# Kernel tuning notes

Measured on AMD Instinct MI355X. Metric: run time of the kernel, lower is better.

Reference implementation:

```python
import jax, jax.numpy as jnp
import numpy as np

T_TRACK = 256   # tracklets per graph
M_DET = 256     # detections per graph
N_NODES = T_TRACK + M_DET
D_IN = 512      # raw node feature dim (stand-in for CNN crop features)
D_EMB = 256     # node embedding dim
SLACK = 0.2
LAM = 5.0
SINK_ITERS = 8


def box_iou(a, b):
    # a, b: [E,4] boxes (x1,y1,x2,y2)
    ix1 = jnp.maximum(a[:, 0], b[:, 0])
    iy1 = jnp.maximum(a[:, 1], b[:, 1])
    ix2 = jnp.minimum(a[:, 2], b[:, 2])
    iy2 = jnp.minimum(a[:, 3], b[:, 3])
    inter = jnp.clip(ix2 - ix1, 0.0) * jnp.clip(iy2 - iy1, 0.0)
    area_a = (a[:, 2] - a[:, 0]) * (a[:, 3] - a[:, 1])
    area_b = (b[:, 2] - b[:, 0]) * (b[:, 3] - b[:, 1])
    return inter / (area_a + area_b - inter + 1e-8)


def mlp2(x, W1, b1, W2, b2):
    return jax.nn.sigmoid(jax.nn.relu(x @ W1 + b1) @ W2 + b2)


def setup_inputs() -> dict:
    key = jax.random.key(0)
    ks = jax.random.split(key, 16)
    x = jax.random.normal(ks[0], (N_NODES, D_IN), jnp.float32)
    coords = jax.random.uniform(ks[1], (N_NODES, 4), jnp.float32)
    # valid boxes: x1<x2, y1<y2
    c = jax.random.uniform(ks[2], (N_NODES, 2), jnp.float32) * 100.0
    wh = jax.random.uniform(ks[3], (N_NODES, 2), jnp.float32) * 20.0 + 1.0
    coords_original = jnp.concatenate([c, c + wh], axis=1)
    # bipartite edges: track i (node i) <-> det j (node T_TRACK+j), both directions;
    # first T*M edges satisfy src < dst (the half kept by the row<col mask)
    src = jnp.repeat(jnp.arange(T_TRACK, dtype=jnp.int32), M_DET)
    dst = jnp.tile(jnp.arange(M_DET, dtype=jnp.int32) + T_TRACK, T_TRACK)
    edge_index = jnp.stack([jnp.concatenate([src, dst]), jnp.concatenate([dst, src])])
    s = 0.05
    p = lambda k, shp: jax.random.normal(k, shp, jnp.float32) * s
    return dict(
        x=x, coords=coords, coords_original=coords_original, edge_index=edge_index,
        W_cnn=p(ks[4], (D_IN, D_EMB)), b_cnn=jnp.zeros((D_EMB,), jnp.float32),
        Wapp1=p(ks[5], (2 * D_EMB, 128)), bapp1=jnp.zeros((128,), jnp.float32),
        Wapp2=p(ks[6], (128, 1)), bapp2=jnp.zeros((1,), jnp.float32),
        Wg1=p(ks[7], (8, 32)), bg1=jnp.zeros((32,), jnp.float32),
        Wg2=p(ks[8], (32, 1)), bg2=jnp.zeros((1,), jnp.float32),
        Wa1=p(ks[9], (2, 8)), ba1=jnp.zeros((8,), jnp.float32),
        Wa2=p(ks[10], (8, 1)), ba2=jnp.zeros((1,), jnp.float32),
        Wo1=p(ks[11], (D_EMB, D_EMB)), Wo2=p(ks[12], (D_EMB, D_EMB)),
        bo=jnp.zeros((D_EMB,), jnp.float32),
        Wf1=p(ks[13], (2, 8)), bf1=jnp.zeros((8,), jnp.float32),
        Wf2=p(ks[14], (8, 1)), bf2=jnp.zeros((1,), jnp.float32),
    )


def reference(x, coords, coords_original, edge_index, W_cnn, b_cnn, Wapp1, bapp1, Wapp2, bapp2, Wg1, bg1, Wg2, bg2, Wa1, ba1, Wa2, ba2, Wo1, Wo2, bo, Wf1, bf1, Wf2, bf2):
    src, dst = edge_index[0], edge_index[1]
    h = jax.nn.relu(x @ W_cnn + b_cnn)                      # [N, D]
    # per-edge appearance / geometry affinities (vectorized over all edges)
    app = mlp2(jnp.concatenate([h[src], h[dst]], 1), Wapp1, bapp1, Wapp2, bapp2)[:, 0]
    geo = mlp2(jnp.concatenate([coords[src], coords[dst]], 1), Wg1, bg1, Wg2, bg2)[:, 0]
    iou = box_iou(coords_original[src], coords_original[dst])
    e = mlp2(jnp.stack([app, geo], -1), Wa1, ba1, Wa2, ba2)[:, 0]   # [E]
    # message passing (optimNet): edge-gated neighbor aggregation
    agg = jax.ops.segment_sum(e[:, None] * h[src], dst, num_segments=N_NODES)
    out = jax.nn.relu(h @ Wo1 + agg @ Wo2 + bo)             # [N, D]
    # directed (src < dst) half of the edges only
    eh = T_TRACK * M_DET
    a, b = out[src[:eh]], out[dst[:eh]]
    na = jnp.maximum(jnp.linalg.norm(a, axis=-1), 1e-6)
    nb = jnp.maximum(jnp.linalg.norm(b, axis=-1), 1e-6)
    cos = jnp.sum(a * b, -1) / (na * nb)
    score = mlp2(jnp.stack([cos, iou[:eh]], -1), Wf1, bf1, Wf2, bf2)[:, 0]
    # assignment matrix with slack row/col, Sinkhorn normalization
    slack_v = jnp.exp(jnp.float32(LAM * SLACK))
    mat = jnp.full((T_TRACK + 1, M_DET + 1), slack_v, jnp.float32)
    mat = mat.at[:T_TRACK, :M_DET].set(jnp.exp(LAM * score).reshape(T_TRACK, M_DET))
    for _ in range(SINK_ITERS):
        mat = mat / jnp.sum(mat, axis=1, keepdims=True)
        mat = mat / jnp.sum(mat, axis=0, keepdims=True)
    return mat[:T_TRACK, :M_DET].reshape(-1)                # [T*M]
```

## Files before the change

### kernel.cpp

```cpp
#include <hip/hip_runtime.h>
#include <math.h>


__device__ __forceinline__ float sigmoidf_(float x) { return 1.0f / (1.0f + expf(-x)); }

typedef _Float16 h2t __attribute__((ext_vector_type(2)));

__device__ __forceinline__ h2t pack2(float x, float y) {
  h2t r; r.x = (_Float16)x; r.y = (_Float16)y; return r;
}
__device__ __forceinline__ float fdot2f(h2t a, h2t b, float c) {
  return __builtin_amdgcn_fdot2(a, b, c, false);
}
template <int CTRL>
__device__ __forceinline__ float dpp_get(float x) {
  return __builtin_bit_cast(
      float, __builtin_amdgcn_mov_dpp(__builtin_bit_cast(int, x), CTRL, 0xF, 0xF, false));
}
template <int IMM>
__device__ __forceinline__ float swz_get(float x) {
  return __builtin_bit_cast(
      float, __builtin_amdgcn_ds_swizzle(__builtin_bit_cast(int, x), IMM));
}
__device__ __forceinline__ float allred16(float x) {
  x += dpp_get<0xB1>(x);
  x += dpp_get<0x4E>(x);
  x += dpp_get<0x141>(x);
  x += dpp_get<0x140>(x);
  return x;
}

#define G_LOAD(T, AREG, BARR, AP, BP, LDB)                             \
  {                                                                    \
    AREG = *reinterpret_cast<const float4*>((AP) + (T) * 32);          \
    _Pragma("unroll") for (int kk = 0; kk < 32; ++kk)                  \
        BARR[kk] = (BP)[((T) * 32 + kk) * (LDB)];                      \
  }
#define G_STORE(BUF, AREG)                                             \
  {                                                                    \
    Ast[BUF][ac + 0][ar] = AREG.x; Ast[BUF][ac + 1][ar] = AREG.y;      \
    Ast[BUF][ac + 2][ar] = AREG.z; Ast[BUF][ac + 3][ar] = AREG.w;      \
  }
#define G_COMP(BUF, BARR)                                              \
  {                                                                    \
    _Pragma("unroll") for (int kk = 0; kk < 32; ++kk) {                \
      const float4 a4 =                                                \
          *reinterpret_cast<const float4*>(&Ast[BUF][kk][4 * ty]);     \
      const float bv = BARR[kk];                                       \
      acc[0] = fmaf(a4.x, bv, acc[0]); acc[1] = fmaf(a4.y, bv, acc[1]);\
      acc[2] = fmaf(a4.z, bv, acc[2]); acc[3] = fmaf(a4.w, bv, acc[3]);\
    }                                                                  \
  }

__global__ __launch_bounds__(256)
void k1_h(const float* __restrict__ x, const float* __restrict__ Wc,
          float* __restrict__ hAB) {
  __shared__ __align__(16) float Ast[2][32][36];
  const int tid = threadIdx.x;
  const int tx = tid & 31, ty = tid >> 5;
  const int ar = tid >> 3, ac = (tid & 7) * 4;
  const int bm = blockIdx.y * 32, bn = blockIdx.x * 32;
  const int z = blockIdx.z;
  const float* __restrict__ Bp = Wc + (z * 256) * 256 + bn + tx;
  const float* __restrict__ Ap = x + (bm + ar) * 512 + z * 256 + ac;
  float* __restrict__ Cout = hAB + z * 131072;
  float4 aA, aB;
  float bA[32], bB[32];
  float acc[4] = {0.f, 0.f, 0.f, 0.f};

  G_LOAD(0, aA, bA, Ap, Bp, 256);
  G_STORE(0, aA);
  __syncthreads();
  for (int t = 0; t < 8; t += 2) {
    G_LOAD(t + 1, aB, bB, Ap, Bp, 256);
    G_COMP(0, bA);
    G_STORE(1, aB);
    __syncthreads();
    if (t + 2 < 8) { G_LOAD(t + 2, aA, bA, Ap, Bp, 256); }
    G_COMP(1, bB);
    if (t + 2 < 8) { G_STORE(0, aA); }
    __syncthreads();
  }
#pragma unroll
  for (int i = 0; i < 4; ++i)
    Cout[(bm + 4 * ty + i) * 256 + bn + tx] = acc[i];
}

__global__ __launch_bounds__(256)
void k2_pqgw(const float* __restrict__ hAB, const float* __restrict__ bc,
             const float* __restrict__ W1, const float* __restrict__ b1,
             const float* __restrict__ Wo2, const float* __restrict__ Wo1,
             float* __restrict__ PQGW, float* __restrict__ PT) {
  __shared__ __align__(16) float Ast[2][32][36];
  const int tid = threadIdx.x;
  const int tx = tid & 31, ty = tid >> 5;
  const int ar = tid >> 3, ac = (tid & 7) * 4;
  const int bm = blockIdx.y * 32, bn = blockIdx.x * 32;
  const int col = bn + tx;
  const float* __restrict__ Bp;
  int ldb;
  if (bn < 128)       { Bp = W1 + col; ldb = 128; }
  else if (bn < 256)  { Bp = W1 + 256 * 128 + (col - 128); ldb = 128; }
  else if (bn < 512)  { Bp = Wo2 + (col - 256); ldb = 256; }
  else                { Bp = Wo1 + (col - 512); ldb = 256; }
  const float* __restrict__ ApA = hAB + (bm + ar) * 256 + ac;
  const float* __restrict__ ApB = ApA + 131072;
  const float* __restrict__ bcp = bc + ac;
  float4 aA, aB;
  float bA[32], bB[32];
  float acc[4] = {0.f, 0.f, 0.f, 0.f};

#define K2_LOAD(T, AREG, BARR)                                         \
  {                                                                    \
    const float4 xa = *reinterpret_cast<const float4*>(ApA + (T) * 32);\
    const float4 xb = *reinterpret_cast<const float4*>(ApB + (T) * 32);\
    const float4 xc = *reinterpret_cast<const float4*>(bcp + (T) * 32);\
    AREG.x = fmaxf(xa.x + xb.x + xc.x, 0.f);                           \
    AREG.y = fmaxf(xa.y + xb.y + xc.y, 0.f);                           \
    AREG.z = fmaxf(xa.z + xb.z + xc.z, 0.f);                           \
    AREG.w = fmaxf(xa.w + xb.w + xc.w, 0.f);                           \
    _Pragma("unroll") for (int kk = 0; kk < 32; ++kk)                  \
        BARR[kk] = Bp[((T) * 32 + kk) * ldb];                          \
  }

  K2_LOAD(0, aA, bA);
  G_STORE(0, aA);
  __syncthreads();
  for (int t = 0; t < 8; t += 2) {
    K2_LOAD(t + 1, aB, bB);
    G_COMP(0, bA);
    G_STORE(1, aB);
    __syncthreads();
    if (t + 2 < 8) { K2_LOAD(t + 2, aA, bA); }
    G_COMP(1, bB);
    if (t + 2 < 8) { G_STORE(0, aA); }
    __syncthreads();
  }
  if (bn < 128) {
    const float bias = b1[col];
#pragma unroll
    for (int i = 0; i < 4; ++i)
      PT[col * 512 + bm + 4 * ty + i] = acc[i] + bias;
  } else {
#pragma unroll
    for (int i = 0; i < 4; ++i)
      PQGW[(bm + 4 * ty + i) * 768 + col] = acc[i];
  }
#undef K2_LOAD
}

__global__ __launch_bounds__(256)
void k34_edges_out(const float* __restrict__ PQGW, const float* __restrict__ PT,
                   const float* __restrict__ coords, const float* __restrict__ Wapp2,
                   const float* __restrict__ bapp2, const float* __restrict__ Wg1,
                   const float* __restrict__ bg1, const float* __restrict__ Wg2,
                   const float* __restrict__ bg2, const float* __restrict__ Wa1,
                   const float* __restrict__ ba1, const float* __restrict__ Wa2,
                   const float* __restrict__ ba2, const float* __restrict__ bo,
                   float* __restrict__ outm, float* __restrict__ nrm) {
  __shared__ __align__(16) float2 qw[128];
  __shared__ __align__(16) float sWg1[256], sWg2[32], sGfix[32];
  __shared__ __align__(16) float sE[256];
  __shared__ float sWa1[16], sBa1[8], sWa2[8], wpart[4];
  const int tid = threadIdx.x;
  const int b = blockIdx.x;
  const bool istrack = (b < 256);
  const int vbase = istrack ? 256 : 0;

  if (tid < 128) {
    float2 t2;
    t2.x = PQGW[b * 768 + 128 + tid];
    t2.y = Wapp2[tid];
    qw[tid] = t2;
  }
  sWg1[tid] = Wg1[tid];
  if (tid < 32) sWg2[tid] = Wg2[tid];
  if (tid < 16) sWa1[tid] = Wa1[tid];
  if (tid < 8) { sBa1[tid] = ba1[tid]; sWa2[tid] = Wa2[tid]; }
  __syncthreads();
  if (tid < 32) {
    float g = bg1[tid];
#pragma unroll
    for (int q = 0; q < 4; ++q)
      g = fmaf(coords[b * 4 + q], sWg1[(4 + q) * 32 + tid], g);
    sGfix[tid] = g;
  }
  __syncthreads();

  const int vr = vbase + tid;
  const float* __restrict__ ptb = PT + vr;
  float z = 0.f;
#pragma unroll 8
  for (int j = 0; j < 128; ++j) {
    const float2 q2 = qw[j];
    float a = ptb[j * 512] + q2.x;
    a = a > 0.f ? a : 0.f;
    z = fmaf(a, q2.y, z);
  }
  const float app = sigmoidf_(z + bapp2[0]);
  const float4 cp = *reinterpret_cast<const float4*>(coords + vr * 4);
  float gz = 0.f;
#pragma unroll
  for (int m = 0; m < 32; ++m) {
    float hm = sGfix[m];
    hm = fmaf(cp.x, sWg1[0 * 32 + m], hm);
    hm = fmaf(cp.y, sWg1[1 * 32 + m], hm);
    hm = fmaf(cp.z, sWg1[2 * 32 + m], hm);
    hm = fmaf(cp.w, sWg1[3 * 32 + m], hm);
    hm = hm > 0.f ? hm : 0.f;
    gz = fmaf(hm, sWg2[m], gz);
  }
  const float geo = sigmoidf_(gz + bg2[0]);
  float ez = 0.f;
#pragma unroll
  for (int m = 0; m < 8; ++m) {
    float hm = fmaf(app, sWa1[m], fmaf(geo, sWa1[8 + m], sBa1[m]));
    hm = hm > 0.f ? hm : 0.f;
    ez = fmaf(hm, sWa2[m], ez);
  }
  sE[tid] = sigmoidf_(ez + ba2[0]);
  __syncthreads();

  const int c = tid;
  float a0 = 0.f, a1 = 0.f, a2 = 0.f, a3 = 0.f;
  const float* __restrict__ gcol = PQGW + vbase * 768 + 256 + c;
#pragma unroll 4
  for (int j = 0; j < 256; j += 4) {
    const float4 e4 = *reinterpret_cast<const float4*>(&sE[j]);
    a0 = fmaf(e4.x, gcol[(j + 0) * 768], a0);
    a1 = fmaf(e4.y, gcol[(j + 1) * 768], a1);
    a2 = fmaf(e4.z, gcol[(j + 2) * 768], a2);
    a3 = fmaf(e4.w, gcol[(j + 3) * 768], a3);
  }
  const float base = PQGW[b * 768 + 512 + c] + bo[c];
  float vv = base + ((a0 + a1) + (a2 + a3));
  vv = vv > 0.f ? vv : 0.f;
  outm[b * 256 + c] = vv;
  float nsq = vv * vv;
  nsq = allred16(nsq);
  nsq += swz_get<0x401F>(nsq);
  nsq += __shfl_xor(nsq, 32, 64);
  if ((tid & 63) == 0) wpart[tid >> 6] = nsq;
  __syncthreads();
  if (tid == 0)
    nrm[b] = fmaxf(sqrtf(wpart[0] + wpart[1] + wpart[2] + wpart[3]), 1e-6f);
}

__global__ __launch_bounds__(256)
void k6_score(const float* __restrict__ outm, const float* __restrict__ nrm,
              const float* __restrict__ co, const float* __restrict__ Wf1,
              const float* __restrict__ bf1, const float* __restrict__ Wf2,
              const float* __restrict__ bf2, float* __restrict__ Mblk) {
  __shared__ __align__(16) float Ast[2][32][36];
  const int tid = threadIdx.x;
  const int tx = tid & 31, ty = tid >> 5;
  const int ar = tid >> 3, ac = (tid & 7) * 4;
  const int s0 = blockIdx.y * 32, d0 = blockIdx.x * 32;
  const float* __restrict__ Ap = outm + (s0 + ar) * 256 + ac;
  const float* __restrict__ Bp = outm + (256 + d0 + tx) * 256;
  float4 aA, aB;
  float bA[32], bB[32];
  float acc[4] = {0.f, 0.f, 0.f, 0.f};

  G_LOAD(0, aA, bA, Ap, Bp, 1);
  G_STORE(0, aA);
  __syncthreads();
  for (int t = 0; t < 8; t += 2) {
    G_LOAD(t + 1, aB, bB, Ap, Bp, 1);
    G_COMP(0, bA);
    G_STORE(1, aB);
    __syncthreads();
    if (t + 2 < 8) { G_LOAD(t + 2, aA, bA, Ap, Bp, 1); }
    G_COMP(1, bB);
    if (t + 2 < 8) { G_STORE(0, aA); }
    __syncthreads();
  }
  const float nb = nrm[256 + d0 + tx];
  const float4 B4 = *reinterpret_cast<const float4*>(co + (256 + d0 + tx) * 4);
  const float areaB = (B4.z - B4.x) * (B4.w - B4.y);
  float w1c[8], w1i[8], w2[8];
#pragma unroll
  for (int m = 0; m < 8; ++m) {
    w1c[m] = Wf1[m]; w1i[m] = Wf1[8 + m]; w2[m] = Wf2[m];
  }
  const float bf20 = bf2[0];
#pragma unroll
  for (int i = 0; i < 4; ++i) {
    const int r = s0 + 4 * ty + i;
    const float4 A4 = *reinterpret_cast<const float4*>(co + r * 4);
    const float ix1 = fmaxf(A4.x, B4.x), iy1 = fmaxf(A4.y, B4.y);
    const float ix2 = fminf(A4.z, B4.z), iy2 = fminf(A4.w, B4.w);
    const float inter = fmaxf(ix2 - ix1, 0.f) * fmaxf(iy2 - iy1, 0.f);
    const float areaA = (A4.z - A4.x) * (A4.w - A4.y);
    const float i1 = inter / (areaA + areaB - inter + 1e-8f);
    const float cosv = acc[i] / (nrm[r] * nb);
    float sz = 0.f;
#pragma unroll
    for (int m = 0; m < 8; ++m) {
      float hm = fmaf(cosv, w1c[m], fmaf(i1, w1i[m], bf1[m]));
      hm = hm > 0.f ? hm : 0.f;
      sz = fmaf(hm, w2[m], sz);
    }
    const float score = sigmoidf_(sz + bf20);
    Mblk[r * 256 + d0 + tx] = expf(5.0f * score);
  }
}

__global__ __launch_bounds__(1024)
void k7_sink(const float* __restrict__ Mg, float* __restrict__ outp) {
  __shared__ __align__(16) float su_f[256];
  __shared__ __align__(16) float svs_f[256];
  __shared__ __align__(16) float psum[16][260];
  __shared__ float wsumU[16], wsumV[4];
  const int tid = threadIdx.x, w = tid >> 6, l = tid & 63;
  const float slack = 2.71828182845904523536f;
  const float INV256 = 0.00390625f;
  const int rev = ((l & 1) << 3) | ((l & 2) << 1) | ((l & 4) >> 1) | ((l & 8) >> 3);
  const bool b0 = l & 1, b1 = l & 2, b2 = l & 4, b3 = l & 8;

  h2t mrA[16], mrB[16];
#pragma unroll
  for (int i = 0; i < 16; ++i) {
    const float4 f = *reinterpret_cast<const float4*>(Mg + (w * 16 + i) * 256 + 4 * l);
    mrA[i] = pack2(f.x, f.y);
    mrB[i] = pack2(f.z, f.w);
  }
  if (tid < 256) svs_f[tid] = 256.0f;
  __syncthreads();

  float sv256 = 1.0f;
  for (int it = 0; it < 8; ++it) {
    const float sv_tot =
        (it == 0) ? 257.0f : (wsumV[0] + wsumV[1] + wsumV[2] + wsumV[3] + sv256);
    const float su256 = 1.0f / (slack * sv_tot);
    const float4 va = *reinterpret_cast<const float4*>(&svs_f[4 * l]);
    const h2t sva = pack2(va.x, va.y), svb = pack2(va.z, va.w);
    float p[16];
#pragma unroll
    for (int i = 0; i < 16; ++i) p[i] = fdot2f(mrA[i], sva, fdot2f(mrB[i], svb, 0.0f));
#pragma unroll
    for (int i = 0; i < 8; ++i) {
      const float keep = b0 ? p[i + 8] : p[i], give = b0 ? p[i] : p[i + 8];
      p[i] = keep + dpp_get<0xB1>(give);
    }
#pragma unroll
    for (int i = 0; i < 4; ++i) {
      const float keep = b1 ? p[i + 4] : p[i], give = b1 ? p[i] : p[i + 4];
      p[i] = keep + dpp_get<0x4E>(give);
    }
#pragma unroll
    for (int i = 0; i < 2; ++i) {
      const float keep = b2 ? p[i + 2] : p[i], give = b2 ? p[i] : p[i + 2];
      p[i] = keep + dpp_get<0x141>(give);
    }
    {
      const float keep = b3 ? p[1] : p[0], give = b3 ? p[0] : p[1];
      p[0] = keep + dpp_get<0x140>(give);
    }
    float S = p[0];
    S += swz_get<0x401F>(S);
    S += __shfl_xor(S, 32, 64);
    const float su_val = 1.0f / (S * INV256 + slack * sv256);
    if (l < 16) su_f[w * 16 + rev] = su_val;
    const float wsU = allred16(su_val);
    if (l == 0) wsumU[w] = wsU;
    asm volatile("s_waitcnt lgkmcnt(0)" ::: "memory");
    float su16[16];
#pragma unroll
    for (int k = 0; k < 16; k += 4) {
      const float4 t = *reinterpret_cast<const float4*>(&su_f[w * 16 + k]);
      su16[k] = t.x; su16[k + 1] = t.y; su16[k + 2] = t.z; su16[k + 3] = t.w;
    }
    float pc0 = 0.f, pc1 = 0.f, pc2 = 0.f, pc3 = 0.f;
#pragma unroll
    for (int i = 0; i < 16; ++i) {
      const float ui = su16[i];
      pc0 = fmaf((float)mrA[i].x, ui, pc0);
      pc1 = fmaf((float)mrA[i].y, ui, pc1);
      pc2 = fmaf((float)mrB[i].x, ui, pc2);
      pc3 = fmaf((float)mrB[i].y, ui, pc3);
    }
    float4 pcv; pcv.x = pc0; pcv.y = pc1; pcv.z = pc2; pcv.w = pc3;
    *reinterpret_cast<float4*>(&psum[w][4 * l]) = pcv;
    __syncthreads();
    const float su_tot = wsumU[0] + wsumU[1] + wsumU[2] + wsumU[3] + wsumU[4] +
                         wsumU[5] + wsumU[6] + wsumU[7] + wsumU[8] + wsumU[9] +
                         wsumU[10] + wsumU[11] + wsumU[12] + wsumU[13] +
                         wsumU[14] + wsumU[15] + su256;
    if (tid < 256) {
      float cs = 0.f;
#pragma unroll
      for (int g = 0; g < 16; ++g) cs += psum[g][tid];
      const float sv_val = 1.0f / (cs + slack * su256);
      svs_f[tid] = 256.0f * sv_val;
      float t = allred16(sv_val);
      t += swz_get<0x401F>(t);
      t += __shfl_xor(t, 32, 64);
      if (l == 0) wsumV[w] = t;
    }
    sv256 = 1.0f / (slack * su_tot);
    __syncthreads();
  }
  const float4 sv4 = *reinterpret_cast<const float4*>(&svs_f[4 * l]);
#pragma unroll
  for (int i = 0; i < 16; ++i) {
    const float uo = su_f[w * 16 + i] * INV256;
    float4 o;
    o.x = uo * (float)mrA[i].x * sv4.x;
    o.y = uo * (float)mrA[i].y * sv4.y;
    o.z = uo * (float)mrB[i].x * sv4.z;
    o.w = uo * (float)mrB[i].y * sv4.w;
    *reinterpret_cast<float4*>(outp + (w * 16 + i) * 256 + 4 * l) = o;
  }
}

extern "C" void kernel_launch(void* const* d_in, const int* in_sizes, int n_in,
                              void* d_out, int out_size, void* d_ws, size_t ws_size,
                              hipStream_t stream) {
  (void)in_sizes; (void)n_in; (void)out_size; (void)ws_size;
  const float* x      = (const float*)d_in[0];
  const float* coords = (const float*)d_in[1];
  const float* co     = (const float*)d_in[2];
  const float* Wc    = (const float*)d_in[4];
  const float* bc    = (const float*)d_in[5];
  const float* Wapp1 = (const float*)d_in[6];
  const float* bapp1 = (const float*)d_in[7];
  const float* Wapp2 = (const float*)d_in[8];
  const float* bapp2 = (const float*)d_in[9];
  const float* Wg1   = (const float*)d_in[10];
  const float* bg1   = (const float*)d_in[11];
  const float* Wg2   = (const float*)d_in[12];
  const float* bg2   = (const float*)d_in[13];
  const float* Wa1   = (const float*)d_in[14];
  const float* ba1   = (const float*)d_in[15];
  const float* Wa2   = (const float*)d_in[16];
  const float* ba2   = (const float*)d_in[17];
  const float* Wo1   = (const float*)d_in[18];
  const float* Wo2   = (const float*)d_in[19];
  const float* bo    = (const float*)d_in[20];
  const float* Wf1   = (const float*)d_in[21];
  const float* bf1   = (const float*)d_in[22];
  const float* Wf2   = (const float*)d_in[23];
  const float* bf2   = (const float*)d_in[24];

  float* ws   = (float*)d_ws;
  float* hAB  = ws + 0;
  float* PQGW = ws + 262144;
  float* PT   = ws + 655360;
  float* outm = ws + 720896;
  float* nrm  = ws + 851968;
  float* Mblk = ws + 852480;

  k1_h<<<dim3(8, 16, 2), 256, 0, stream>>>(x, Wc, hAB);
  k2_pqgw<<<dim3(24, 16), 256, 0, stream>>>(hAB, bc, Wapp1, bapp1, Wo2, Wo1,
                                            PQGW, PT);
  k34_edges_out<<<512, 256, 0, stream>>>(PQGW, PT, coords, Wapp2, bapp2, Wg1,
                                         bg1, Wg2, bg2, Wa1, ba1, Wa2, ba2, bo,
                                         outm, nrm);
  k6_score<<<dim3(8, 8), 256, 0, stream>>>(outm, nrm, co, Wf1, bf1, Wf2, bf2,
                                           Mblk);
  k7_sink<<<1, 1024, 0, stream>>>(Mblk, (float*)d_out);
}
```

Baseline: 88.66 us.

## Fuse edge/out and score kernels with per-node release/acquire flags

Merges the per-node edge-gating/aggregation kernel and the cosine/IoU score GEMM kernel into one launch of 576 blocks. Score blocks spin on per-node flags, written with release semantics by the producer blocks, so each score tile starts as soon as its 64 rows are ready rather than waiting at a kernel boundary. The flags are reset inside the preceding kernel. This saves a launch gap and lets the two stages overlap. It relies on the producer blocks being scheduled before, or alongside, the spinning consumer blocks. Higher block indices run last in practice, but nothing guarantees it, so there is a deadlock risk, and spinning occupies compute units.

```diff
diff --git a/kernel.cpp b/kernel.cpp
--- a/kernel.cpp
+++ b/kernel.cpp
@@ -90,9 +90,12 @@
 void k2_pqgw(const float* __restrict__ hAB, const float* __restrict__ bc,
              const float* __restrict__ W1, const float* __restrict__ b1,
              const float* __restrict__ Wo2, const float* __restrict__ Wo1,
-             float* __restrict__ PQGW, float* __restrict__ PT) {
+             float* __restrict__ PQGW, float* __restrict__ PT,
+             unsigned* __restrict__ flags) {
   __shared__ __align__(16) float Ast[2][32][36];
   const int tid = threadIdx.x;
+  if (blockIdx.x == 0 && blockIdx.y < 2)
+    flags[(blockIdx.y * 256 + tid) * 16] = 0u;
   const int tx = tid & 31, ty = tid >> 5;
   const int ar = tid >> 3, ac = (tid & 7) * 4;
   const int bm = blockIdx.y * 32, bn = blockIdx.x * 32;
@@ -150,159 +153,179 @@
 }
 
 __global__ __launch_bounds__(256)
-void k34_edges_out(const float* __restrict__ PQGW, const float* __restrict__ PT,
-                   const float* __restrict__ coords, const float* __restrict__ Wapp2,
-                   const float* __restrict__ bapp2, const float* __restrict__ Wg1,
-                   const float* __restrict__ bg1, const float* __restrict__ Wg2,
-                   const float* __restrict__ bg2, const float* __restrict__ Wa1,
-                   const float* __restrict__ ba1, const float* __restrict__ Wa2,
-                   const float* __restrict__ ba2, const float* __restrict__ bo,
-                   float* __restrict__ outm, float* __restrict__ nrm) {
-  __shared__ __align__(16) float2 qw[128];
-  __shared__ __align__(16) float sWg1[256], sWg2[32], sGfix[32];
-  __shared__ __align__(16) float sE[256];
-  __shared__ float sWa1[16], sBa1[8], sWa2[8], wpart[4];
+void k346(const float* __restrict__ PQGW, const float* __restrict__ PT,
+          const float* __restrict__ coords, const float* __restrict__ co,
+          const float* __restrict__ Wapp2, const float* __restrict__ bapp2,
+          const float* __restrict__ Wg1, const float* __restrict__ bg1,
+          const float* __restrict__ Wg2, const float* __restrict__ bg2,
+          const float* __restrict__ Wa1, const float* __restrict__ ba1,
+          const float* __restrict__ Wa2, const float* __restrict__ ba2,
+          const float* __restrict__ bo, const float* __restrict__ Wf1,
+          const float* __restrict__ bf1, const float* __restrict__ Wf2,
+          const float* __restrict__ bf2, float* __restrict__ outm,
+          float* __restrict__ nrm, float* __restrict__ Mblk,
+          unsigned* __restrict__ flags) {
+  __shared__ __align__(16) float smem[2304];
   const int tid = threadIdx.x;
-  const int b = blockIdx.x;
-  const bool istrack = (b < 256);
-  const int vbase = istrack ? 256 : 0;
-
-  if (tid < 128) {
-    float2 t2;
-    t2.x = PQGW[b * 768 + 128 + tid];
-    t2.y = Wapp2[tid];
-    qw[tid] = t2;
-  }
-  sWg1[tid] = Wg1[tid];
-  if (tid < 32) sWg2[tid] = Wg2[tid];
-  if (tid < 16) sWa1[tid] = Wa1[tid];
-  if (tid < 8) { sBa1[tid] = ba1[tid]; sWa2[tid] = Wa2[tid]; }
-  __syncthreads();
-  if (tid < 32) {
-    float g = bg1[tid];
-#pragma unroll
-    for (int q = 0; q < 4; ++q)
-      g = fmaf(coords[b * 4 + q], sWg1[(4 + q) * 32 + tid], g);
-    sGfix[tid] = g;
-  }
-  __syncthreads();
-
-  const int vr = vbase + tid;
-  const float* __restrict__ ptb = PT + vr;
-  float z = 0.f;
+
+  if (blockIdx.x < 512) {
+    float2* qw = reinterpret_cast<float2*>(smem);
+    float* sWg1 = smem + 256;
+    float* sWg2 = smem + 512;
+    float* sGfix = smem + 544;
+    float* sWa1 = smem + 576;
+    float* sBa1 = smem + 592;
+    float* sWa2 = smem + 600;
+    float* wpart = smem + 608;
+    float* sE = smem + 616;
+    const int b = blockIdx.x;
+    const bool istrack = (b < 256);
+    const int vbase = istrack ? 256 : 0;
+
+    if (tid < 128) {
+      float2 t2;
+      t2.x = PQGW[b * 768 + 128 + tid];
+      t2.y = Wapp2[tid];
+      qw[tid] = t2;
+    }
+    sWg1[tid] = Wg1[tid];
+    if (tid < 32) sWg2[tid] = Wg2[tid];
+    if (tid < 16) sWa1[tid] = Wa1[tid];
+    if (tid < 8) { sBa1[tid] = ba1[tid]; sWa2[tid] = Wa2[tid]; }
+    __syncthreads();
+    if (tid < 32) {
+      float g = bg1[tid];
+#pragma unroll
+      for (int q = 0; q < 4; ++q)
+        g = fmaf(coords[b * 4 + q], sWg1[(4 + q) * 32 + tid], g);
+      sGfix[tid] = g;
+    }
+    __syncthreads();
+
+    const int vr = vbase + tid;
+    const float* __restrict__ ptb = PT + vr;
+    float z = 0.f;
 #pragma unroll 8
-  for (int j = 0; j < 128; ++j) {
-    const float2 q2 = qw[j];
-    float a = ptb[j * 512] + q2.x;
-    a = a > 0.f ? a : 0.f;
-    z = fmaf(a, q2.y, z);
-  }
-  const float app = sigmoidf_(z + bapp2[0]);
-  const float4 cp = *reinterpret_cast<const float4*>(coords + vr * 4);
-  float gz = 0.f;
-#pragma unroll
-  for (int m = 0; m < 32; ++m) {
-    float hm = sGfix[m];
-    hm = fmaf(cp.x, sWg1[0 * 32 + m], hm);
-    hm = fmaf(cp.y, sWg1[1 * 32 + m], hm);
-    hm = fmaf(cp.z, sWg1[2 * 32 + m], hm);
-    hm = fmaf(cp.w, sWg1[3 * 32 + m], hm);
-    hm = hm > 0.f ? hm : 0.f;
-    gz = fmaf(hm, sWg2[m], gz);
-  }
-  const float geo = sigmoidf_(gz + bg2[0]);
-  float ez = 0.f;
-#pragma unroll
-  for (int m = 0; m < 8; ++m) {
-    float hm = fmaf(app, sWa1[m], fmaf(geo, sWa1[8 + m], sBa1[m]));
-    hm = hm > 0.f ? hm : 0.f;
-    ez = fmaf(hm, sWa2[m], ez);
-  }
-  sE[tid] = sigmoidf_(ez + ba2[0]);
-  __syncthreads();
-
-  const int c = tid;
-  float a0 = 0.f, a1 = 0.f, a2 = 0.f, a3 = 0.f;
-  const float* __restrict__ gcol = PQGW + vbase * 768 + 256 + c;
+    for (int j = 0; j < 128; ++j) {
+      const float2 q2 = qw[j];
+      float a = ptb[j * 512] + q2.x;
+      a = a > 0.f ? a : 0.f;
+      z = fmaf(a, q2.y, z);
+    }
+    const float app = sigmoidf_(z + bapp2[0]);
+    const float4 cp = *reinterpret_cast<const float4*>(coords + vr * 4);
+    float gz = 0.f;
+#pragma unroll
+    for (int m = 0; m < 32; ++m) {
+      float hm = sGfix[m];
+      hm = fmaf(cp.x, sWg1[0 * 32 + m], hm);
+      hm = fmaf(cp.y, sWg1[1 * 32 + m], hm);
+      hm = fmaf(cp.z, sWg1[2 * 32 + m], hm);
+      hm = fmaf(cp.w, sWg1[3 * 32 + m], hm);
+      hm = hm > 0.f ? hm : 0.f;
+      gz = fmaf(hm, sWg2[m], gz);
+    }
+    const float geo = sigmoidf_(gz + bg2[0]);
+    float ez = 0.f;
+#pragma unroll
+    for (int m = 0; m < 8; ++m) {
+      float hm = fmaf(app, sWa1[m], fmaf(geo, sWa1[8 + m], sBa1[m]));
+      hm = hm > 0.f ? hm : 0.f;
+      ez = fmaf(hm, sWa2[m], ez);
+    }
+    sE[tid] = sigmoidf_(ez + ba2[0]);
+    __syncthreads();
+
+    const int c = tid;
+    float a0 = 0.f, a1 = 0.f, a2 = 0.f, a3 = 0.f;
+    const float* __restrict__ gcol = PQGW + vbase * 768 + 256 + c;
 #pragma unroll 4
-  for (int j = 0; j < 256; j += 4) {
-    const float4 e4 = *reinterpret_cast<const float4*>(&sE[j]);
-    a0 = fmaf(e4.x, gcol[(j + 0) * 768], a0);
-    a1 = fmaf(e4.y, gcol[(j + 1) * 768], a1);
-    a2 = fmaf(e4.z, gcol[(j + 2) * 768], a2);
-    a3 = fmaf(e4.w, gcol[(j + 3) * 768], a3);
-  }
-  const float base = PQGW[b * 768 + 512 + c] + bo[c];
-  float vv = base + ((a0 + a1) + (a2 + a3));
-  vv = vv > 0.f ? vv : 0.f;
-  outm[b * 256 + c] = vv;
-  float nsq = vv * vv;
-  nsq = allred16(nsq);
-  nsq += swz_get<0x401F>(nsq);
-  nsq += __shfl_xor(nsq, 32, 64);
-  if ((tid & 63) == 0) wpart[tid >> 6] = nsq;
-  __syncthreads();
-  if (tid == 0)
-    nrm[b] = fmaxf(sqrtf(wpart[0] + wpart[1] + wpart[2] + wpart[3]), 1e-6f);
-}
-
-__global__ __launch_bounds__(256)
-void k6_score(const float* __restrict__ outm, const float* __restrict__ nrm,
-              const float* __restrict__ co, const float* __restrict__ Wf1,
-              const float* __restrict__ bf1, const float* __restrict__ Wf2,
-              const float* __restrict__ bf2, float* __restrict__ Mblk) {
-  __shared__ __align__(16) float Ast[2][32][36];
-  const int tid = threadIdx.x;
-  const int tx = tid & 31, ty = tid >> 5;
-  const int ar = tid >> 3, ac = (tid & 7) * 4;
-  const int s0 = blockIdx.y * 32, d0 = blockIdx.x * 32;
-  const float* __restrict__ Ap = outm + (s0 + ar) * 256 + ac;
-  const float* __restrict__ Bp = outm + (256 + d0 + tx) * 256;
-  float4 aA, aB;
-  float bA[32], bB[32];
-  float acc[4] = {0.f, 0.f, 0.f, 0.f};
-
-  G_LOAD(0, aA, bA, Ap, Bp, 1);
-  G_STORE(0, aA);
-  __syncthreads();
-  for (int t = 0; t < 8; t += 2) {
-    G_LOAD(t + 1, aB, bB, Ap, Bp, 1);
-    G_COMP(0, bA);
-    G_STORE(1, aB);
-    __syncthreads();
-    if (t + 2 < 8) { G_LOAD(t + 2, aA, bA, Ap, Bp, 1); }
-    G_COMP(1, bB);
-    if (t + 2 < 8) { G_STORE(0, aA); }
-    __syncthreads();
-  }
-  const float nb = nrm[256 + d0 + tx];
-  const float4 B4 = *reinterpret_cast<const float4*>(co + (256 + d0 + tx) * 4);
-  const float areaB = (B4.z - B4.x) * (B4.w - B4.y);
-  float w1c[8], w1i[8], w2[8];
-#pragma unroll
-  for (int m = 0; m < 8; ++m) {
-    w1c[m] = Wf1[m]; w1i[m] = Wf1[8 + m]; w2[m] = Wf2[m];
-  }
-  const float bf20 = bf2[0];
-#pragma unroll
-  for (int i = 0; i < 4; ++i) {
-    const int r = s0 + 4 * ty + i;
-    const float4 A4 = *reinterpret_cast<const float4*>(co + r * 4);
-    const float ix1 = fmaxf(A4.x, B4.x), iy1 = fmaxf(A4.y, B4.y);
-    const float ix2 = fminf(A4.z, B4.z), iy2 = fminf(A4.w, B4.w);
-    const float inter = fmaxf(ix2 - ix1, 0.f) * fmaxf(iy2 - iy1, 0.f);
-    const float areaA = (A4.z - A4.x) * (A4.w - A4.y);
-    const float i1 = inter / (areaA + areaB - inter + 1e-8f);
-    const float cosv = acc[i] / (nrm[r] * nb);
-    float sz = 0.f;
+    for (int j = 0; j < 256; j += 4) {
+      const float4 e4 = *reinterpret_cast<const float4*>(&sE[j]);
+      a0 = fmaf(e4.x, gcol[(j + 0) * 768], a0);
+      a1 = fmaf(e4.y, gcol[(j + 1) * 768], a1);
+      a2 = fmaf(e4.z, gcol[(j + 2) * 768], a2);
+      a3 = fmaf(e4.w, gcol[(j + 3) * 768], a3);
+    }
+    const float base = PQGW[b * 768 + 512 + c] + bo[c];
+    float vv = base + ((a0 + a1) + (a2 + a3));
+    vv = vv > 0.f ? vv : 0.f;
+    outm[b * 256 + c] = vv;
+    float nsq = vv * vv;
+    nsq = allred16(nsq);
+    nsq += swz_get<0x401F>(nsq);
+    nsq += __shfl_xor(nsq, 32, 64);
+    if ((tid & 63) == 0) wpart[tid >> 6] = nsq;
+    __syncthreads();
+    if (tid == 0) {
+      nrm[b] = fmaxf(sqrtf(wpart[0] + wpart[1] + wpart[2] + wpart[3]), 1e-6f);
+      __threadfence();
+      __hip_atomic_store(flags + b * 16, 1u, __ATOMIC_RELEASE,
+                         __HIP_MEMORY_SCOPE_AGENT);
+    }
+  } else {
+    float (*Ast)[32][36] = reinterpret_cast<float (*)[32][36]>(smem);
+    const int bq = blockIdx.x - 512;
+    const int s0 = (bq >> 3) * 32, d0 = (bq & 7) * 32;
+    if (tid < 64) {
+      const unsigned* fp =
+          flags + (tid < 32 ? (s0 + tid) : (256 + d0 + tid - 32)) * 16;
+      while (__hip_atomic_load(fp, __ATOMIC_RELAXED, __HIP_MEMORY_SCOPE_AGENT) == 0)
+        __builtin_amdgcn_s_sleep(8);
+      __threadfence();
+    }
+    __syncthreads();
+
+    const int tx = tid & 31, ty = tid >> 5;
+    const int ar = tid >> 3, ac = (tid & 7) * 4;
+    const float* __restrict__ Ap = outm + (s0 + ar) * 256 + ac;
+    const float* __restrict__ Bp = outm + (256 + d0 + tx) * 256;
+    float4 aA, aB;
+    float bA[32], bB[32];
+    float acc[4] = {0.f, 0.f, 0.f, 0.f};
+
+    G_LOAD(0, aA, bA, Ap, Bp, 1);
+    G_STORE(0, aA);
+    __syncthreads();
+    for (int t = 0; t < 8; t += 2) {
+      G_LOAD(t + 1, aB, bB, Ap, Bp, 1);
+      G_COMP(0, bA);
+      G_STORE(1, aB);
+      __syncthreads();
+      if (t + 2 < 8) { G_LOAD(t + 2, aA, bA, Ap, Bp, 1); }
+      G_COMP(1, bB);
+      if (t + 2 < 8) { G_STORE(0, aA); }
+      __syncthreads();
+    }
+    const float nb = nrm[256 + d0 + tx];
+    const float4 B4 = *reinterpret_cast<const float4*>(co + (256 + d0 + tx) * 4);
+    const float areaB = (B4.z - B4.x) * (B4.w - B4.y);
+    float w1c[8], w1i[8], w2[8];
 #pragma unroll
     for (int m = 0; m < 8; ++m) {
-      float hm = fmaf(cosv, w1c[m], fmaf(i1, w1i[m], bf1[m]));
-      hm = hm > 0.f ? hm : 0.f;
-      sz = fmaf(hm, w2[m], sz);
-    }
-    const float score = sigmoidf_(sz + bf20);
-    Mblk[r * 256 + d0 + tx] = expf(5.0f * score);
+      w1c[m] = Wf1[m]; w1i[m] = Wf1[8 + m]; w2[m] = Wf2[m];
+    }
+    const float bf20 = bf2[0];
+#pragma unroll
+    for (int i = 0; i < 4; ++i) {
+      const int r = s0 + 4 * ty + i;
+      const float4 A4 = *reinterpret_cast<const float4*>(co + r * 4);
+      const float ix1 = fmaxf(A4.x, B4.x), iy1 = fmaxf(A4.y, B4.y);
+      const float ix2 = fminf(A4.z, B4.z), iy2 = fminf(A4.w, B4.w);
+      const float inter = fmaxf(ix2 - ix1, 0.f) * fmaxf(iy2 - iy1, 0.f);
+      const float areaA = (A4.z - A4.x) * (A4.w - A4.y);
+      const float i1 = inter / (areaA + areaB - inter + 1e-8f);
+      const float cosv = acc[i] / (nrm[r] * nb);
+      float sz = 0.f;
+#pragma unroll
+      for (int m = 0; m < 8; ++m) {
+        float hm = fmaf(cosv, w1c[m], fmaf(i1, w1i[m], bf1[m]));
+        hm = hm > 0.f ? hm : 0.f;
+        sz = fmaf(hm, w2[m], sz);
+      }
+      const float score = sigmoidf_(sz + bf20);
+      Mblk[r * 256 + d0 + tx] = expf(5.0f * score);
+    }
   }
 }
 
@@ -450,14 +473,13 @@
   float* outm = ws + 720896;
   float* nrm  = ws + 851968;
   float* Mblk = ws + 852480;
+  unsigned* flags = (unsigned*)(ws + 918016);
 
   k1_h<<<dim3(8, 16, 2), 256, 0, stream>>>(x, Wc, hAB);
   k2_pqgw<<<dim3(24, 16), 256, 0, stream>>>(hAB, bc, Wapp1, bapp1, Wo2, Wo1,
-                                            PQGW, PT);
-  k34_edges_out<<<512, 256, 0, stream>>>(PQGW, PT, coords, Wapp2, bapp2, Wg1,
-                                         bg1, Wg2, bg2, Wa1, ba1, Wa2, ba2, bo,
-                                         outm, nrm);
-  k6_score<<<dim3(8, 8), 256, 0, stream>>>(outm, nrm, co, Wf1, bf1, Wf2, bf2,
-                                           Mblk);
+                                            PQGW, PT, flags);
+  k346<<<576, 256, 0, stream>>>(PQGW, PT, coords, co, Wapp2, bapp2, Wg1, bg1,
+                                Wg2, bg2, Wa1, ba1, Wa2, ba2, bo, Wf1, bf1,
+                                Wf2, bf2, outm, nrm, Mblk, flags);
   k7_sink<<<1, 1024, 0, stream>>>(Mblk, (float*)d_out);
 }
```

New measurement: 116.6 us. 31.5% more time.
